# Kernel optimization log

Measured on AMD Instinct MI355X. Metric: run time of the kernel, lower is better.

## Reference

```python
import jax, jax.numpy as jnp
import numpy as np

TAU = 2.0          # LIF tau
V_TH = 1.0         # threshold, v_reset = 0
EPS = 1e-5         # BN eps
NUM_HEADS = 12
PATCH = 4
LENTH = 64         # (H/p)*(W/p)


def _heaviside(x):
    return (x >= 0.0).astype(x.dtype)


def lif(x_seq):
    """Multi-step LIF (decay_input=True, hard reset to 0). x_seq: [T, ...] -> spikes [T, ...]."""
    def step(v, x):
        v = v + (x - v) / TAU
        s = _heaviside(v - V_TH)
        v = v * (1.0 - s)
        return v, s
    _, s_seq = jax.lax.scan(step, jnp.zeros_like(x_seq[0]), x_seq)
    return s_seq


def bn_eval(x, gamma, beta, mean, var):
    # x: [T,B,C,H,W]; eval-mode BN over channel axis 2
    sh = (1, 1, -1, 1, 1)
    inv = gamma.reshape(sh) / jnp.sqrt(var.reshape(sh) + EPS)
    return (x - mean.reshape(sh)) * inv + beta.reshape(sh)


def setup_inputs() -> dict:
    key = jax.random.key(0)
    ks = jax.random.split(key, 8)
    T, B, C, H, W = 4, 8, 384, 32, 32
    p = PATCH
    x = jax.random.normal(ks[0], (T, B, C, H, W), jnp.float32)
    w_conv = jax.random.normal(ks[1], (2 * C, C, p, p), jnp.float32) / np.sqrt(C * p * p)
    w_proj = jax.random.normal(ks[2], (C, C), jnp.float32) / np.sqrt(C)
    bn1_gamma = 0.5 + jax.random.uniform(ks[3], (2 * C,), jnp.float32)
    bn1_beta = 0.1 * jax.random.normal(ks[4], (2 * C,), jnp.float32)
    bn1_mean = 0.1 * jax.random.normal(ks[5], (2 * C,), jnp.float32)
    bn1_var = 0.5 + jax.random.uniform(ks[6], (2 * C,), jnp.float32)
    bn2_gamma = 0.5 + jax.random.uniform(jax.random.fold_in(key, 10), (C,), jnp.float32)
    bn2_beta = 0.1 * jax.random.normal(jax.random.fold_in(key, 11), (C,), jnp.float32)
    bn2_mean = 0.1 * jax.random.normal(jax.random.fold_in(key, 12), (C,), jnp.float32)
    bn2_var = 0.5 + jax.random.uniform(jax.random.fold_in(key, 13), (C,), jnp.float32)
    fr_x = 0.05 + 0.5 * jax.random.uniform(jax.random.fold_in(key, 14), (1, 1, NUM_HEADS, 1, 1), jnp.float32)
    fr_attn = 0.05 + 0.5 * jax.random.uniform(jax.random.fold_in(key, 15), (1, 1, NUM_HEADS, 1, 1), jnp.float32)
    return dict(x=x, w_conv=w_conv, bn1_gamma=bn1_gamma, bn1_beta=bn1_beta,
                bn1_mean=bn1_mean, bn1_var=bn1_var, w_proj=w_proj,
                bn2_gamma=bn2_gamma, bn2_beta=bn2_beta, bn2_mean=bn2_mean,
                bn2_var=bn2_var, fr_x=fr_x, fr_attn=fr_attn)


def reference(x, w_conv, bn1_gamma, bn1_beta, bn1_mean, bn1_var, w_proj,
              bn2_gamma, bn2_beta, bn2_mean, bn2_var, fr_x, fr_attn):
    T, B, C, H, W = x.shape
    h = NUM_HEADS
    Ch = C // h
    p = PATCH
    x_feat = x
    xs = lif(x)                                           # [T,B,C,H,W] spikes
    # patchify conv (kernel=stride=p, no bias), flatten T*B for the conv
    y = jax.lax.conv_general_dilated(
        xs.reshape(T * B, C, H, W), w_conv, (p, p), 'VALID',
        dimension_numbers=('NCHW', 'OIHW', 'NCHW'))
    Hp, Wp = H // p, W // p
    y = bn_eval(y.reshape(T, B, 2 * C, Hp, Wp), bn1_gamma, bn1_beta, bn1_mean, bn1_var)
    y = y.reshape(T, B, h, 2 * Ch, Hp * Wp)
    y1, y2 = y[:, :, :, :Ch, :], y[:, :, :, Ch:, :]       # [T,B,h,Ch,N']
    xr = xs.reshape(T, B, h, Ch, H * W)                   # [T,B,h,Ch,N]
    scale1 = 1.0 / jnp.sqrt(fr_x * Ch)                    # [1,1,h,1,1]
    attn = jnp.einsum('tbhdp,tbhdn->tbhpn', y1, xr) * scale1   # [T,B,h,N',N]
    attn = lif(attn)
    scale2 = 1.0 / jnp.sqrt(fr_attn * LENTH)
    out = jnp.einsum('tbhdp,tbhpn->tbhdn', y2, attn) * scale2  # [T,B,h,Ch,N]
    out = lif(out.reshape(T, B, C, H, W))
    out = jnp.einsum('tbchw,oc->tbohw', out, w_proj)      # 1x1 conv, no bias
    out = bn_eval(out, bn2_gamma, bn2_beta, bn2_mean, bn2_var)
    return out + x_feat
```

## Files before the change

kernel.cpp:

```cpp
#include <hip/hip_runtime.h>
#include <math.h>

#define TT 4
#define BB 8
#define CC 384
#define HWN 1024
#define NHEAD 12
#define CHD 32
#define C2 768
#define LL 64
#define KCONV 6144
#define KB_TOT 192
#define MROWS 2048

#define K2INV ((_Float16)4.8828125e-4f)

typedef _Float16 f16x8 __attribute__((ext_vector_type(8)));
typedef _Float16 f16x4 __attribute__((ext_vector_type(4)));
typedef float f32x4 __attribute__((ext_vector_type(4)));

#if defined(__has_builtin)
#if __has_builtin(__builtin_amdgcn_global_load_lds)
#define USE_GLL 1
#endif
#endif
#ifndef USE_GLL
#define USE_GLL 0
#endif

#if USE_GLL
typedef __attribute__((address_space(3))) unsigned int lds_uint;
typedef const __attribute__((address_space(1))) unsigned int glob_uint;
__device__ __forceinline__ void load_lds16(const void* g, void* l) {
    __builtin_amdgcn_global_load_lds((glob_uint*)g, (lds_uint*)l, 16, 0, 0);
}
#endif

__global__ __launch_bounds__(256) void k_pack(const float* __restrict__ w,
                                              _Float16* __restrict__ W0,
                                              _Float16* __restrict__ W1) {
    int g = blockIdx.x * 256 + threadIdx.x;
    int o = g * 8;
    int kbnb = o >> 12;
    int kb = kbnb / 6;
    int nb = kbnb - kb * 6;
    int q = (o >> 10) & 3;
    int col = (o >> 3) & 127;
    int k = kb * 32 + q * 8;
    int n = nb * 128 + col;
    const float* src = w + (size_t)n * KCONV + k;
    f16x8 h, l;
#pragma unroll
    for (int j = 0; j < 8; j++) {
        float wv = src[j];
        _Float16 hi = (_Float16)wv;
        float rem = (wv - (float)hi) * 2048.0f;
        h[j] = hi;
        l[j] = (_Float16)rem;
    }
    *(f16x8*)(W0 + o) = h;
    *(f16x8*)(W1 + o) = l;
}

__global__ __launch_bounds__(256) void k_pack_wp(const float* __restrict__ wp,
                                                 _Float16* __restrict__ WpH) {
    int g = blockIdx.x * 256 + threadIdx.x;
    int o8 = g * 8;
    int kbot = o8 >> 12;
    int kb = kbot / 3;
    int ot = kbot - kb * 3;
    int q = (o8 >> 10) & 3;
    int row = (o8 >> 3) & 127;
    int o = ot * 128 + row;
    int c = kb * 32 + q * 8;
    const float* src = wp + (size_t)o * CC + c;
    f16x8 h;
#pragma unroll
    for (int j = 0; j < 8; j++) h[j] = (_Float16)src[j];
    *(f16x8*)(WpH + o8) = h;
}

__global__ __launch_bounds__(256) void k_lif1(const float* __restrict__ x,
                                              _Float16* __restrict__ xsC,
                                              _Float16* __restrict__ xsF) {
    int nt = blockIdx.x & 3, q8 = blockIdx.x >> 2;
    int bh = blockIdx.y;
    int b = bh / NHEAD, hh = bh % NHEAD;
    int n = nt * 256 + threadIdx.x;
    const int stride = BB * CC * HWN;
    int h = n >> 5, w = n & 31;
    int pi = h >> 2, a = h & 3, pj = w >> 2, bp = w & 3;
    int rowp = pi * 8 + pj;
    int qa = a >> 1;
    int jc = (a & 1) * 4 + bp;
    size_t base0 = ((size_t)b * CC + hh * 32 + q8 * 8) * HWN + n;
    f16x8 frag[4];
#pragma unroll
    for (int j = 0; j < 8; j++) {
        int c = hh * 32 + q8 * 8 + j;
        int kb = c >> 1;
        int qc = (c & 1) * 2 + qa;
        size_t cbase = (size_t)kb * 4096 + qc * 1024 + jc;
        float v = 0.0f;
        size_t off = base0 + (size_t)j * HWN;
#pragma unroll
        for (int t = 0; t < TT; t++) {
            float xv = x[(size_t)t * stride + off];
            v += (xv - v) * 0.5f;
            float s = (v >= 1.0f) ? 1.0f : 0.0f;
            if (s > 0.0f) v = 0.0f;
            frag[t][j] = (_Float16)s;
            int tb = t * BB + b;
            int mt = tb >> 1;
            int row = (tb & 1) * 64 + rowp;
            xsC[(size_t)mt * (192 * 4096) + cbase + (size_t)row * 8] = (_Float16)s;
        }
    }
#pragma unroll
    for (int t = 0; t < TT; t++) {
        int tb = t * BB + b;
        size_t dst = ((size_t)(tb * NHEAD + hh) * 8 + (n >> 7)) * 4096 + q8 * 1024 + (size_t)(n & 127) * 8;
        *(f16x8*)(xsF + dst) = frag[t];
    }
}

__global__ __launch_bounds__(256, 2) void k_conv_mfma(const _Float16* __restrict__ xsC,
                                                      const _Float16* __restrict__ W0,
                                                      const _Float16* __restrict__ W1,
                                                      float* __restrict__ P,
                                                      int kbPerSplit) {
    __shared__ __align__(16) _Float16 As[2][4096];
    __shared__ __align__(16) _Float16 Bh[2][4096];
    __shared__ __align__(16) _Float16 Bl[2][4096];

    int mt = blockIdx.x;
    int nt = blockIdx.y;
    int s = blockIdx.z;
    int kb0 = s * kbPerSplit;
    int tid = threadIdx.x;
    int wave = tid >> 6;
    int lane = tid & 63;
    int l16 = lane & 15, lq = lane >> 4;
    int wr = (wave & 1) * 64, wc = (wave >> 1) * 64;

    f32x4 acc[4][4];
#pragma unroll
    for (int i = 0; i < 4; i++)
#pragma unroll
        for (int j = 0; j < 4; j++) acc[i][j] = (f32x4){0.f, 0.f, 0.f, 0.f};

    const char* aBase = (const char*)xsC + (size_t)mt * (192 * 8192);
    const char* b0Base = (const char*)W0 + (size_t)nt * 8192;
    const char* b1Base = (const char*)W1 + (size_t)nt * 8192;
    int wo = wave * 2048;
    int lo16 = lane * 16;

#if USE_GLL
#define STAGE(buf, kb) do {                                              \
    const char* aS = aBase + (size_t)(kb) * 8192;                        \
    const char* b0S = b0Base + (size_t)(kb) * (6 * 8192);                \
    const char* b1S = b1Base + (size_t)(kb) * (6 * 8192);                \
    load_lds16(aS + wo + lo16, (char*)As[buf] + wo);                     \
    load_lds16(aS + wo + 1024 + lo16, (char*)As[buf] + wo + 1024);       \
    load_lds16(b0S + wo + lo16, (char*)Bh[buf] + wo);                    \
    load_lds16(b0S + wo + 1024 + lo16, (char*)Bh[buf] + wo + 1024);      \
    load_lds16(b1S + wo + lo16, (char*)Bl[buf] + wo);                    \
    load_lds16(b1S + wo + 1024 + lo16, (char*)Bl[buf] + wo + 1024);      \
} while (0)
#else
#define STAGE(buf, kb) do {                                              \
    const char* aS = aBase + (size_t)(kb) * 8192;                        \
    const char* b0S = b0Base + (size_t)(kb) * (6 * 8192);                \
    const char* b1S = b1Base + (size_t)(kb) * (6 * 8192);                \
    _Pragma("unroll")                                                    \
    for (int i_ = 0; i_ < 2; ++i_) {                                     \
        int off_ = wo + i_ * 1024 + lo16;                                \
        *(float4*)((char*)As[buf] + off_) = *(const float4*)(aS + off_); \
        *(float4*)((char*)Bh[buf] + off_) = *(const float4*)(b0S + off_);\
        *(float4*)((char*)Bl[buf] + off_) = *(const float4*)(b1S + off_);\
    }                                                                    \
} while (0)
#endif

    STAGE(0, kb0);
    __syncthreads();

    int cur = 0;
    for (int i = 0; i < kbPerSplit; ++i) {
        if (i + 1 < kbPerSplit) STAGE(cur ^ 1, kb0 + i + 1);

        f16x8 wf[4], sf[4], sfs[4];
#pragma unroll
        for (int fj = 0; fj < 4; fj++) {
            sf[fj] = *(const f16x8*)&As[cur][(size_t)(lq * 128 + wr + fj * 16 + l16) * 8];
            sfs[fj] = sf[fj] * K2INV;
        }
#pragma unroll
        for (int fi = 0; fi < 4; fi++)
            wf[fi] = *(const f16x8*)&Bh[cur][(size_t)(lq * 128 + wc + fi * 16 + l16) * 8];
#pragma unroll
        for (int fi = 0; fi < 4; fi++)
#pragma unroll
            for (int fj = 0; fj < 4; fj++)
                acc[fi][fj] = __builtin_amdgcn_mfma_f32_16x16x32_f16(wf[fi], sf[fj], acc[fi][fj], 0, 0, 0);
#pragma unroll
        for (int fi = 0; fi < 4; fi++)
            wf[fi] = *(const f16x8*)&Bl[cur][(size_t)(lq * 128 + wc + fi * 16 + l16) * 8];
#pragma unroll
        for (int fi = 0; fi < 4; fi++)
#pragma unroll
            for (int fj = 0; fj < 4; fj++)
                acc[fi][fj] = __builtin_amdgcn_mfma_f32_16x16x32_f16(wf[fi], sfs[fj], acc[fi][fj], 0, 0, 0);

        __syncthreads();
        cur ^= 1;
    }
#undef STAGE

    size_t Pbase = (size_t)s * MROWS * C2;
#pragma unroll
    for (int fi = 0; fi < 4; fi++) {
        int oc0 = nt * 128 + wc + fi * 16 + lq * 4;
#pragma unroll
        for (int fj = 0; fj < 4; fj++) {
            int m = mt * 128 + wr + fj * 16 + l16;
            *(f32x4*)(P + Pbase + (size_t)m * C2 + oc0) = acc[fi][fj];
        }
    }
}

__global__ __launch_bounds__(256) void k_reduce_frag(const float* __restrict__ P,
                                                     const float* __restrict__ g1,
                                                     const float* __restrict__ b1,
                                                     const float* __restrict__ m1,
                                                     const float* __restrict__ v1,
                                                     _Float16* __restrict__ A1,
                                                     _Float16* __restrict__ A2,
                                                     int KS) {
    __shared__ float y2ls[32][66];
    int tb = blockIdx.x / NHEAD, hh = blockIdx.x % NHEAD;
    int tid = threadIdx.x;
    int pp = tid >> 2, cq = (tid & 3) * 16;

    size_t rowbase = ((size_t)tb * 64 + pp) * C2 + hh * 64 + cq;
    float yv[16];
#pragma unroll
    for (int i = 0; i < 16; i++) yv[i] = 0.0f;
    for (int s = 0; s < KS; s++) {
        const float* p = P + (size_t)s * MROWS * C2 + rowbase;
#pragma unroll
        for (int i4 = 0; i4 < 4; i4++) {
            float4 v = *(const float4*)(p + i4 * 4);
            yv[i4 * 4 + 0] += v.x;
            yv[i4 * 4 + 1] += v.y;
            yv[i4 * 4 + 2] += v.z;
            yv[i4 * 4 + 3] += v.w;
        }
    }
#pragma unroll
    for (int i = 0; i < 16; i++) {
        int oc = hh * 64 + cq + i;
        float inv = g1[oc] / sqrtf(v1[oc] + 1e-5f);
        yv[i] = (yv[i] - m1[oc]) * inv + b1[oc];
    }

    size_t reg = (size_t)(tb * NHEAD + hh) * 4096;
    if (cq < 32) {
#pragma unroll
        for (int gi = 0; gi < 2; gi++) {
            int c0 = cq + gi * 8;
            f16x8 h, l;
#pragma unroll
            for (int j = 0; j < 8; j++) {
                float v = yv[gi * 8 + j];
                _Float16 hi = (_Float16)v;
                h[j] = hi;
                l[j] = (_Float16)((v - (float)hi) * 2048.0f);
            }
            size_t a = reg + (size_t)(((pp >> 4) * 4 + (c0 >> 3)) * 128 + (pp & 15) * 8);
            *(f16x8*)(A1 + a) = h;
            *(f16x8*)(A1 + a + 2048) = l;
        }
    } else {
#pragma unroll
        for (int i = 0; i < 16; i++) y2ls[cq - 32 + i][pp] = yv[i];
    }
    __syncthreads();
    int d16 = tid & 15, grp = tid >> 4;
    f16x8 h, l;
#pragma unroll
    for (int j = 0; j < 8; j++) {
        float v = y2ls[(grp >> 3) * 16 + d16][((grp >> 2) & 1) * 32 + (grp & 3) * 8 + j];
        _Float16 hi = (_Float16)v;
        h[j] = hi;
        l[j] = (_Float16)((v - (float)hi) * 2048.0f);
    }
    size_t a = reg + (size_t)((grp * 16 + d16) * 8);
    *(f16x8*)(A2 + a) = h;
    *(f16x8*)(A2 + a + 2048) = l;
}

__global__ __launch_bounds__(256) void k_attn_mfma(const _Float16* __restrict__ xsF,
                                                   const _Float16* __restrict__ A1,
                                                   const _Float16* __restrict__ A2,
                                                   const float* __restrict__ fr_x,
                                                   const float* __restrict__ fr_attn,
                                                   _Float16* __restrict__ OsF) {
    __shared__ __align__(16) _Float16 Bs[4][128][8];
    __shared__ __align__(16) _Float16 Sat[8][128][8];

    int nt = blockIdx.x;
    int bh = blockIdx.y;
    int b = bh / NHEAD, hh = bh % NHEAD;
    int tid = threadIdx.x;
    int w = tid >> 6;
    int lane = tid & 63;
    int l16 = lane & 15, lq = lane >> 4;

    float scale1 = 1.0f / sqrtf(fr_x[hh] * 32.0f);
    float scale2 = 1.0f / sqrtf(fr_attn[hh] * 64.0f);

    float va[8][4];
    float vo[2][2][4];
#pragma unroll
    for (int nf = 0; nf < 8; nf++)
#pragma unroll
        for (int r = 0; r < 4; r++) va[nf][r] = 0.0f;
#pragma unroll
    for (int dt = 0; dt < 2; dt++)
#pragma unroll
        for (int nf = 0; nf < 2; nf++)
#pragma unroll
            for (int r = 0; r < 4; r++) vo[dt][nf][r] = 0.0f;

    for (int t = 0; t < TT; t++) {
        int tb = t * BB + b;
        size_t reg = (size_t)(tb * NHEAD + hh);
        const char* src = (const char*)(xsF + (reg * 8 + nt) * 4096);
#if USE_GLL
        load_lds16(src + tid * 16, (char*)&Bs[0][0][0] + tid * 16);
        load_lds16(src + tid * 16 + 4096, (char*)&Bs[0][0][0] + tid * 16 + 4096);
#else
        *(float4*)((char*)&Bs[0][0][0] + tid * 16) = *(const float4*)(src + tid * 16);
        *(float4*)((char*)&Bs[0][0][0] + tid * 16 + 4096) = *(const float4*)(src + tid * 16 + 4096);
#endif
        const _Float16* a1b = A1 + reg * 4096;
        f16x8 a1h = *(const f16x8*)(a1b + (size_t)(((w * 4 + lq) * 16 + l16) * 8));
        f16x8 a1l = *(const f16x8*)(a1b + 2048 + (size_t)(((w * 4 + lq) * 16 + l16) * 8));
        f16x8 a1ls = a1l * K2INV;
        __syncthreads();

        f32x4 ah[8];
#pragma unroll
        for (int nf = 0; nf < 8; nf++) ah[nf] = (f32x4){0.f, 0.f, 0.f, 0.f};
#pragma unroll
        for (int nf = 0; nf < 8; nf++) {
            f16x8 bf = *(const f16x8*)&Bs[lq][nf * 16 + l16][0];
            ah[nf] = __builtin_amdgcn_mfma_f32_16x16x32_f16(a1h, bf, ah[nf], 0, 0, 0);
            ah[nf] = __builtin_amdgcn_mfma_f32_16x16x32_f16(a1ls, bf, ah[nf], 0, 0, 0);
        }
        int pq = w * 2 + (lq >> 1);
#pragma unroll
        for (int nf = 0; nf < 8; nf++) {
            f16x4 sp;
#pragma unroll
            for (int r = 0; r < 4; r++) {
                float a = ah[nf][r] * scale1;
                float v = va[nf][r];
                v += (a - v) * 0.5f;
                float s = (v >= 1.0f) ? 1.0f : 0.0f;
                va[nf][r] = (s > 0.0f) ? 0.0f : v;
                sp[r] = (_Float16)s;
            }
            *(f16x4*)&Sat[pq][nf * 16 + l16][(lq & 1) * 4] = sp;
        }
        __syncthreads();

        const _Float16* a2b = A2 + reg * 4096;
        f32x4 oh[2][2];
#pragma unroll
        for (int dt = 0; dt < 2; dt++)
#pragma unroll
            for (int nf = 0; nf < 2; nf++) oh[dt][nf] = (f32x4){0.f, 0.f, 0.f, 0.f};
#pragma unroll
        for (int ks = 0; ks < 2; ks++) {
            f16x8 bf0 = *(const f16x8*)&Sat[ks * 4 + lq][w * 32 + l16][0];
            f16x8 bf1 = *(const f16x8*)&Sat[ks * 4 + lq][w * 32 + 16 + l16][0];
#pragma unroll
            for (int dt = 0; dt < 2; dt++) {
                size_t ao = (size_t)(((dt * 8 + ks * 4 + lq) * 16 + l16) * 8);
                f16x8 a2h = *(const f16x8*)(a2b + ao);
                f16x8 a2ls = *(const f16x8*)(a2b + 2048 + ao) * K2INV;
                oh[dt][0] = __builtin_amdgcn_mfma_f32_16x16x32_f16(a2h, bf0, oh[dt][0], 0, 0, 0);
                oh[dt][0] = __builtin_amdgcn_mfma_f32_16x16x32_f16(a2ls, bf0, oh[dt][0], 0, 0, 0);
                oh[dt][1] = __builtin_amdgcn_mfma_f32_16x16x32_f16(a2h, bf1, oh[dt][1], 0, 0, 0);
                oh[dt][1] = __builtin_amdgcn_mfma_f32_16x16x32_f16(a2ls, bf1, oh[dt][1], 0, 0, 0);
            }
        }
        _Float16* og = OsF + (reg * 8 + nt) * 4096;
#pragma unroll
        for (int dt = 0; dt < 2; dt++)
#pragma unroll
            for (int nf = 0; nf < 2; nf++) {
                f16x4 sp;
#pragma unroll
                for (int r = 0; r < 4; r++) {
                    float a = oh[dt][nf][r] * scale2;
                    float v = vo[dt][nf][r];
                    v += (a - v) * 0.5f;
                    float s = (v >= 1.0f) ? 1.0f : 0.0f;
                    vo[dt][nf][r] = (s > 0.0f) ? 0.0f : v;
                    sp[r] = (_Float16)s;
                }
                int n = w * 32 + nf * 16 + l16;
                *(f16x4*)(og + (size_t)((dt * 2 + (lq >> 1)) * 1024 + n * 8 + (lq & 1) * 4)) = sp;
            }
        __syncthreads();
    }
}

__global__ __launch_bounds__(256, 2) void k_proj_mfma(const _Float16* __restrict__ OsF,
                                                      const _Float16* __restrict__ WpH,
                                                      const float* __restrict__ g2,
                                                      const float* __restrict__ b2,
                                                      const float* __restrict__ m2,
                                                      const float* __restrict__ vv2,
                                                      const float* __restrict__ x,
                                                      float* __restrict__ out) {
    __shared__ __align__(16) _Float16 Bs[2][4096];

    int nt = blockIdx.x;
    int ot = blockIdx.y;
    int tb = blockIdx.z;
    int tid = threadIdx.x;
    int wave = tid >> 6;
    int lane = tid & 63;
    int l16 = lane & 15, lq = lane >> 4;
    int wn = (wave & 1) * 64, wo = (wave >> 1) * 64;

    f32x4 acc[4][4];
#pragma unroll
    for (int i = 0; i < 4; i++)
#pragma unroll
        for (int j = 0; j < 4; j++) acc[i][j] = (f32x4){0.f, 0.f, 0.f, 0.f};

    const char* bBase = (const char*)(OsF + ((size_t)tb * NHEAD * 8 + nt) * 4096);
    const _Float16* aBase = WpH + (size_t)ot * 4096 + lq * 1024 + (size_t)(wo + l16) * 8;
    int halfo = wave * 2048;
    int lo16 = lane * 16;

#if USE_GLL
#define PSTAGE(buf, kb) do {                                                   \
    const char* bS = bBase + (size_t)(kb) * (8 * 8192);                        \
    load_lds16(bS + halfo + lo16, (char*)Bs[buf] + halfo);                     \
    load_lds16(bS + halfo + 1024 + lo16, (char*)Bs[buf] + halfo + 1024);       \
} while (0)
#else
#define PSTAGE(buf, kb) do {                                                   \
    const char* bS = bBase + (size_t)(kb) * (8 * 8192);                        \
    _Pragma("unroll")                                                          \
    for (int i_ = 0; i_ < 2; ++i_) {                                           \
        int off_ = halfo + i_ * 1024 + lo16;                                   \
        *(float4*)((char*)Bs[buf] + off_) = *(const float4*)(bS + off_);       \
    }                                                                          \
} while (0)
#endif

    f16x8 af[4], afn[4];
#pragma unroll
    for (int fo = 0; fo < 4; fo++) af[fo] = *(const f16x8*)(aBase + (size_t)(fo * 16) * 8);
    PSTAGE(0, 0);
    __syncthreads();

    int cur = 0;
    for (int kb = 0; kb < 12; ++kb) {
        int kbn = (kb + 1 < 12) ? kb + 1 : kb;
        if (kb + 1 < 12) PSTAGE(cur ^ 1, kb + 1);
        const _Float16* an = aBase + (size_t)kbn * (3 * 4096);
#pragma unroll
        for (int fo = 0; fo < 4; fo++) afn[fo] = *(const f16x8*)(an + (size_t)(fo * 16) * 8);

        f16x8 bf[4];
#pragma unroll
        for (int fn = 0; fn < 4; fn++)
            bf[fn] = *(const f16x8*)&Bs[cur][(size_t)(lq * 128 + wn + fn * 16 + l16) * 8];
#pragma unroll
        for (int fn = 0; fn < 4; fn++)
#pragma unroll
            for (int fo = 0; fo < 4; fo++)
                acc[fn][fo] = __builtin_amdgcn_mfma_f32_16x16x32_f16(bf[fn], af[fo], acc[fn][fo], 0, 0, 0);

        __syncthreads();
        cur ^= 1;
#pragma unroll
        for (int fo = 0; fo < 4; fo++) af[fo] = afn[fo];
    }
#undef PSTAGE

    size_t orow_base = (size_t)tb * CC * HWN;
#pragma unroll
    for (int fo = 0; fo < 4; fo++) {
        int o = ot * 128 + wo + fo * 16 + l16;
        float inv = g2[o] / sqrtf(vv2[o] + 1e-5f);
        float mu = m2[o];
        float bt = b2[o];
        size_t obase = orow_base + (size_t)o * HWN;
#pragma unroll
        for (int fn = 0; fn < 4; fn++) {
            size_t addr = obase + (size_t)(nt * 128 + wn + fn * 16 + lq * 4);
            float4 xv = *(const float4*)(x + addr);
            f32x4 a = acc[fn][fo];
            float4 ov;
            ov.x = (a[0] - mu) * inv + bt + xv.x;
            ov.y = (a[1] - mu) * inv + bt + xv.y;
            ov.z = (a[2] - mu) * inv + bt + xv.z;
            ov.w = (a[3] - mu) * inv + bt + xv.w;
            *(float4*)(out + addr) = ov;
        }
    }
}

extern "C" void kernel_launch(void* const* d_in, const int* in_sizes, int n_in,
                              void* d_out, int out_size, void* d_ws, size_t ws_size,
                              hipStream_t stream) {
    const float* x = (const float*)d_in[0];
    const float* w_conv = (const float*)d_in[1];
    const float* bn1_gamma = (const float*)d_in[2];
    const float* bn1_beta = (const float*)d_in[3];
    const float* bn1_mean = (const float*)d_in[4];
    const float* bn1_var = (const float*)d_in[5];
    const float* w_proj = (const float*)d_in[6];
    const float* bn2_gamma = (const float*)d_in[7];
    const float* bn2_beta = (const float*)d_in[8];
    const float* bn2_mean = (const float*)d_in[9];
    const float* bn2_var = (const float*)d_in[10];
    const float* fr_x = (const float*)d_in[11];
    const float* fr_attn = (const float*)d_in[12];

    const size_t FRAG = (size_t)16 * 192 * 4096 * 2;
    const size_t AB = (size_t)TT * BB * NHEAD * 4096 * 2;
    const size_t WB = (size_t)KCONV * C2 * 2;
    const size_t WPB = (size_t)CC * CC * 2;
    const size_t PB = (size_t)MROWS * C2 * 4;
    _Float16* xsC = (_Float16*)d_ws;
    _Float16* xsF = (_Float16*)((char*)xsC + FRAG);
    _Float16* OsF = (_Float16*)((char*)xsF + FRAG);
    _Float16* A1 = (_Float16*)((char*)OsF + FRAG);
    _Float16* A2 = (_Float16*)((char*)A1 + AB);
    _Float16* W0 = (_Float16*)((char*)A2 + AB);
    _Float16* W1 = (_Float16*)((char*)W0 + WB);
    _Float16* WpH = (_Float16*)((char*)W1 + WB);
    char* tail = (char*)WpH + WPB;

    int KS;
    float* P;
    if (ws_size >= (size_t)(tail - (char*)d_ws) + 8 * PB) {
        KS = 8;
        P = (float*)tail;
    } else if (ws_size >= (size_t)(tail - (char*)d_ws) + 4 * PB) {
        KS = 4;
        P = (float*)tail;
    } else {
        KS = 2;
        P = (float*)OsF;
    }
    int kbPerSplit = KB_TOT / KS;

    k_pack<<<(KCONV * C2 / 8) / 256, 256, 0, stream>>>(w_conv, W0, W1);
    k_pack_wp<<<(CC * CC / 8) / 256, 256, 0, stream>>>(w_proj, WpH);
    k_lif1<<<dim3(16, BB * NHEAD), 256, 0, stream>>>(x, xsC, xsF);
    k_conv_mfma<<<dim3(16, 6, KS), 256, 0, stream>>>(xsC, W0, W1, P, kbPerSplit);
    k_reduce_frag<<<32 * NHEAD, 256, 0, stream>>>(P, bn1_gamma, bn1_beta, bn1_mean, bn1_var, A1, A2, KS);
    k_attn_mfma<<<dim3(8, BB * NHEAD), 256, 0, stream>>>(xsF, A1, A2, fr_x, fr_attn, OsF);
    k_proj_mfma<<<dim3(8, 3, 32), 256, 0, stream>>>(OsF, WpH, bn2_gamma, bn2_beta, bn2_mean, bn2_var, x, (float*)d_out);
}
```

Before: 131.1 us.

## Coalesce weight packing via LDS staging and remap conv/proj block order for XCD locality

The weight pack kernels now read fp32 weights with coalesced float4 row loads, stage the fp16 hi/lo results in shared memory, and write contiguous 16-element chunks, where before each thread did eight strided scalar reads. The conv GEMM grid is flattened so split-K slices of one output tile get adjacent block IDs. The projection grid is remapped so blocks sharing a tb land on the same XCD (bid&7), aiming at better L2 reuse of the OsF and x data. This adds index arithmetic and an LDS round trip plus a barrier in the pack kernels.

```diff
diff --git a/kernel.cpp b/kernel.cpp
--- a/kernel.cpp
+++ b/kernel.cpp
@@ -39,45 +39,57 @@
 __global__ __launch_bounds__(256) void k_pack(const float* __restrict__ w,
                                               _Float16* __restrict__ W0,
                                               _Float16* __restrict__ W1) {
-    int g = blockIdx.x * 256 + threadIdx.x;
-    int o = g * 8;
-    int kbnb = o >> 12;
-    int kb = kbnb / 6;
-    int nb = kbnb - kb * 6;
-    int q = (o >> 10) & 3;
-    int col = (o >> 3) & 127;
-    int k = kb * 32 + q * 8;
-    int n = nb * 128 + col;
-    const float* src = w + (size_t)n * KCONV + k;
-    f16x8 h, l;
-#pragma unroll
-    for (int j = 0; j < 8; j++) {
-        float wv = src[j];
-        _Float16 hi = (_Float16)wv;
-        float rem = (wv - (float)hi) * 2048.0f;
-        h[j] = hi;
-        l[j] = (_Float16)rem;
-    }
-    *(f16x8*)(W0 + o) = h;
-    *(f16x8*)(W1 + o) = l;
+    __shared__ __align__(16) _Float16 Lh[4096];
+    __shared__ __align__(16) _Float16 Ll[4096];
+    int kb = blockIdx.x, nb = blockIdx.y;
+    int tid = threadIdx.x;
+    int r0 = tid >> 3;
+    int c4 = (tid & 7) * 4;
+    int q = c4 >> 3, j0 = c4 & 7;
+#pragma unroll
+    for (int ri = 0; ri < 4; ri++) {
+        int col = ri * 32 + r0;
+        const float* src = w + (size_t)(nb * 128 + col) * KCONV + kb * 32 + c4;
+        float4 v = *(const float4*)src;
+        float vv[4] = {v.x, v.y, v.z, v.w};
+#pragma unroll
+        for (int e = 0; e < 4; e++) {
+            _Float16 h = (_Float16)vv[e];
+            float rem = (vv[e] - (float)h) * 2048.0f;
+            Lh[q * 1024 + col * 8 + j0 + e] = h;
+            Ll[q * 1024 + col * 8 + j0 + e] = (_Float16)rem;
+        }
+    }
+    __syncthreads();
+    size_t o = ((size_t)kb * 6 + nb) * 4096 + tid * 16;
+    *(f16x8*)(W0 + o) = *(const f16x8*)&Lh[tid * 16];
+    *(f16x8*)(W0 + o + 8) = *(const f16x8*)&Lh[tid * 16 + 8];
+    *(f16x8*)(W1 + o) = *(const f16x8*)&Ll[tid * 16];
+    *(f16x8*)(W1 + o + 8) = *(const f16x8*)&Ll[tid * 16 + 8];
 }
 
 __global__ __launch_bounds__(256) void k_pack_wp(const float* __restrict__ wp,
                                                  _Float16* __restrict__ WpH) {
-    int g = blockIdx.x * 256 + threadIdx.x;
-    int o8 = g * 8;
-    int kbot = o8 >> 12;
-    int kb = kbot / 3;
-    int ot = kbot - kb * 3;
-    int q = (o8 >> 10) & 3;
-    int row = (o8 >> 3) & 127;
-    int o = ot * 128 + row;
-    int c = kb * 32 + q * 8;
-    const float* src = wp + (size_t)o * CC + c;
-    f16x8 h;
-#pragma unroll
-    for (int j = 0; j < 8; j++) h[j] = (_Float16)src[j];
-    *(f16x8*)(WpH + o8) = h;
+    __shared__ __align__(16) _Float16 Lh[4096];
+    int kb = blockIdx.x, ot = blockIdx.y;
+    int tid = threadIdx.x;
+    int r0 = tid >> 3;
+    int c4 = (tid & 7) * 4;
+    int q = c4 >> 3, j0 = c4 & 7;
+#pragma unroll
+    for (int ri = 0; ri < 4; ri++) {
+        int col = ri * 32 + r0;
+        const float* src = wp + (size_t)(ot * 128 + col) * CC + kb * 32 + c4;
+        float4 v = *(const float4*)src;
+        float vv[4] = {v.x, v.y, v.z, v.w};
+#pragma unroll
+        for (int e = 0; e < 4; e++)
+            Lh[q * 1024 + col * 8 + j0 + e] = (_Float16)vv[e];
+    }
+    __syncthreads();
+    size_t o = ((size_t)kb * 3 + ot) * 4096 + tid * 16;
+    *(f16x8*)(WpH + o) = *(const f16x8*)&Lh[tid * 16];
+    *(f16x8*)(WpH + o + 8) = *(const f16x8*)&Lh[tid * 16 + 8];
 }
 
 __global__ __launch_bounds__(256) void k_lif1(const float* __restrict__ x,
@@ -128,14 +140,16 @@
                                                       const _Float16* __restrict__ W0,
                                                       const _Float16* __restrict__ W1,
                                                       float* __restrict__ P,
-                                                      int kbPerSplit) {
+                                                      int KS, int kbPerSplit) {
     __shared__ __align__(16) _Float16 As[2][4096];
     __shared__ __align__(16) _Float16 Bh[2][4096];
     __shared__ __align__(16) _Float16 Bl[2][4096];
 
-    int mt = blockIdx.x;
-    int nt = blockIdx.y;
-    int s = blockIdx.z;
+    int bid = blockIdx.x;
+    int s = bid % KS;
+    int idx = bid / KS;
+    int mt = idx & 15;
+    int nt = idx >> 4;
     int kb0 = s * kbPerSplit;
     int tid = threadIdx.x;
     int wave = tid >> 6;
@@ -429,9 +443,13 @@
                                                       float* __restrict__ out) {
     __shared__ __align__(16) _Float16 Bs[2][4096];
 
-    int nt = blockIdx.x;
-    int ot = blockIdx.y;
-    int tb = blockIdx.z;
+    int bid = blockIdx.x;
+    int xcd = bid & 7;
+    int idx = bid >> 3;
+    int tb = xcd * 4 + idx / 24;
+    int rem = idx % 24;
+    int nt = rem & 7;
+    int ot = rem >> 3;
     int tid = threadIdx.x;
     int wave = tid >> 6;
     int lane = tid & 63;
@@ -566,11 +584,11 @@
     }
     int kbPerSplit = KB_TOT / KS;
 
-    k_pack<<<(KCONV * C2 / 8) / 256, 256, 0, stream>>>(w_conv, W0, W1);
-    k_pack_wp<<<(CC * CC / 8) / 256, 256, 0, stream>>>(w_proj, WpH);
+    k_pack<<<dim3(KB_TOT, 6), 256, 0, stream>>>(w_conv, W0, W1);
+    k_pack_wp<<<dim3(12, 3), 256, 0, stream>>>(w_proj, WpH);
     k_lif1<<<dim3(16, BB * NHEAD), 256, 0, stream>>>(x, xsC, xsF);
-    k_conv_mfma<<<dim3(16, 6, KS), 256, 0, stream>>>(xsC, W0, W1, P, kbPerSplit);
+    k_conv_mfma<<<96 * KS, 256, 0, stream>>>(xsC, W0, W1, P, KS, kbPerSplit);
     k_reduce_frag<<<32 * NHEAD, 256, 0, stream>>>(P, bn1_gamma, bn1_beta, bn1_mean, bn1_var, A1, A2, KS);
     k_attn_mfma<<<dim3(8, BB * NHEAD), 256, 0, stream>>>(xsF, A1, A2, fr_x, fr_attn, OsF);
-    k_proj_mfma<<<dim3(8, 3, 32), 256, 0, stream>>>(OsF, WpH, bn2_gamma, bn2_beta, bn2_mean, bn2_var, x, (float*)d_out);
-}
+    k_proj_mfma<<<768, 256, 0, stream>>>(OsF, WpH, bn2_gamma, bn2_beta, bn2_mean, bn2_var, x, (float*)d_out);
+}
```

After: 124.5 us. -5.1%, faster.
